# Optimization experiments

Measured on AMD Instinct MI355X. Metric: run time of the kernel, lower is better.

The kernel has to match this reference:

```python
import jax, jax.numpy as jnp
import numpy as np

D_MODEL = 1024
N_HEADS = 16
D_K = D_MODEL // N_HEADS


def setup_inputs() -> dict:
    key = jax.random.key(0)
    ks = jax.random.split(key, 10)
    s = 1.0 / np.sqrt(D_MODEL)
    def lin(k):
        kw, kb = jax.random.split(k)
        W = jax.random.uniform(kw, (D_MODEL, D_MODEL), jnp.float32, -s, s)
        b = jax.random.uniform(kb, (D_MODEL,), jnp.float32, -s, s)
        return W, b
    Wq, bq = lin(ks[0])
    Wk, bk = lin(ks[1])
    Wv, bv = lin(ks[2])
    Wo, bo = lin(ks[3])
    x = jax.random.normal(ks[4], (2, 2048, D_MODEL), jnp.float32)
    gamma = jnp.ones((D_MODEL,), jnp.float32)
    beta = jnp.zeros((D_MODEL,), jnp.float32)
    return {"x": x, "Wq": Wq, "bq": bq, "Wk": Wk, "bk": bk,
            "Wv": Wv, "bv": bv, "Wo": Wo, "bo": bo,
            "gamma": gamma, "beta": beta}


def _mha(x, Wq, bq, Wk, bk, Wv, bv, Wo, bo, gamma, beta):
    B, S, _ = x.shape
    residual = x
    # Linear uses y = x @ W.T + b (torch nn.Linear convention)
    q = (x @ Wq.T + bq).reshape(B, S, N_HEADS, D_K).transpose(0, 2, 1, 3)
    k = (x @ Wk.T + bk).reshape(B, S, N_HEADS, D_K).transpose(0, 2, 1, 3)
    v = (x @ Wv.T + bv).reshape(B, S, N_HEADS, D_K).transpose(0, 2, 1, 3)
    scores = jnp.einsum("bhqd,bhkd->bhqk", q, k) / jnp.sqrt(jnp.float32(D_K))
    attn = jax.nn.softmax(scores, axis=-1)
    out = jnp.einsum("bhqk,bhkd->bhqd", attn, v)
    out = out.transpose(0, 2, 1, 3).reshape(B, S, D_MODEL)
    out = out @ Wo.T + bo
    h = out + residual
    mu = jnp.mean(h, axis=-1, keepdims=True)
    var = jnp.var(h, axis=-1, keepdims=True)
    h = (h - mu) / jnp.sqrt(var + 1e-5) * gamma + beta
    return jnp.where(h >= 0, h, 0.01 * h)


def reference(x, Wq, bq, Wk, bk, Wv, bv, Wo, bo, gamma, beta):
    return _mha(x, Wq, bq, Wk, bk, Wv, bv, Wo, bo, gamma, beta)
```

## Files before the change

### kernel.cpp

```cpp
#include <hip/hip_runtime.h>

#define DM   1024
#define NH   16
#define DK   64
#define SEQ  2048
#define BATCH 2

typedef __attribute__((ext_vector_type(8))) short bf16x8;
typedef __attribute__((ext_vector_type(4))) float f32x4;

__device__ __forceinline__ unsigned short f2bf(float f) {
    unsigned int u = __builtin_bit_cast(unsigned int, f);
    u += 0x7FFFu + ((u >> 16) & 1u);
    return (unsigned short)(u >> 16);
}

__global__ __launch_bounds__(256)
void cvt_kernel(const float* __restrict__ x,
                const float* __restrict__ wq, const float* __restrict__ wk,
                const float* __restrict__ wv, const float* __restrict__ wo,
                unsigned short* __restrict__ xb,
                unsigned short* __restrict__ wqkvb,
                unsigned short* __restrict__ wob)
{
    const int seg = blockIdx.y;
    const float* src;
    unsigned short* dst;
    int n;
    if (seg == 0)      { src = x;  dst = xb;                  n = 4 << 20; }
    else if (seg == 1) { src = wq; dst = wqkvb;               n = 1 << 20; }
    else if (seg == 2) { src = wk; dst = wqkvb + (1 << 20);   n = 1 << 20; }
    else if (seg == 3) { src = wv; dst = wqkvb + (2 << 20);   n = 1 << 20; }
    else               { src = wo; dst = wob;                 n = 1 << 20; }
    for (int i = (blockIdx.x * 256 + threadIdx.x) * 4; i < n; i += 1024 * 256 * 4) {
        const float4 v = *reinterpret_cast<const float4*>(&src[i]);
        ushort4 o;
        o.x = f2bf(v.x); o.y = f2bf(v.y); o.z = f2bf(v.z); o.w = f2bf(v.w);
        *reinterpret_cast<ushort4*>(&dst[i]) = o;
    }
}

template <int MODE, int BN>
__global__ __launch_bounds__(256)
void gemm2_kernel(const unsigned short* __restrict__ Ab,
                  const unsigned short* __restrict__ Wall,
                  const float* __restrict__ B0, const float* __restrict__ B1,
                  const float* __restrict__ B2,
                  unsigned short* __restrict__ q_ws,
                  unsigned short* __restrict__ k_ws,
                  unsigned short* __restrict__ vt_ws,
                  const float* __restrict__ resid,
                  float* __restrict__ h_ws)
{
    __shared__ unsigned short sA[128 * 32];
    __shared__ unsigned short sB[BN * 32];

    const int tid = threadIdx.x, lane = tid & 63, wid = tid >> 6;
    const int n0 = blockIdx.x * BN, m0 = blockIdx.y * 128;
    const int z  = (MODE == 0) ? blockIdx.z : 0;
    const unsigned short* W = Wall + (size_t)z * (1 << 20);
    const float* bias = (MODE == 0) ? (z == 0 ? B0 : (z == 1 ? B1 : B2)) : B0;

    const int g = lane >> 4, lq = lane & 15;
    const int wr = wid >> 1, wc = wid & 1;
    const int rA = lane >> 2;
    const int csh = (lane & 3) * 8;

    f32x4 acc[4][BN / 32] = {};

    for (int k0 = 0; k0 < DM; k0 += 32) {
        #pragma unroll
        for (int i = 0; i < 2; ++i) {
            const int c = wid * 2 + i;
            __builtin_amdgcn_global_load_lds(
                (const __attribute__((address_space(1))) unsigned int*)
                    &Ab[(size_t)(m0 + c * 16 + rA) * DM + k0 + csh],
                (__attribute__((address_space(3))) unsigned int*)&sA[c * 512],
                16, 0, 0);
        }
        #pragma unroll
        for (int i = 0; i < BN / 64; ++i) {
            const int c = wid * (BN / 64) + i;
            __builtin_amdgcn_global_load_lds(
                (const __attribute__((address_space(1))) unsigned int*)
                    &W[(size_t)(n0 + c * 16 + rA) * DM + k0 + csh],
                (__attribute__((address_space(3))) unsigned int*)&sB[c * 512],
                16, 0, 0);
        }
        __syncthreads();

        bf16x8 a[4], b[BN / 32];
        #pragma unroll
        for (int m = 0; m < 4; ++m)
            a[m] = *reinterpret_cast<const bf16x8*>(&sA[(wr * 64 + m * 16 + lq) * 32 + 8 * g]);
        #pragma unroll
        for (int n = 0; n < BN / 32; ++n)
            b[n] = *reinterpret_cast<const bf16x8*>(&sB[(wc * (BN / 2) + n * 16 + lq) * 32 + 8 * g]);
        #pragma unroll
        for (int m = 0; m < 4; ++m)
            #pragma unroll
            for (int n = 0; n < BN / 32; ++n)
                acc[m][n] = __builtin_amdgcn_mfma_f32_16x16x32_bf16(
                    a[m], b[n], acc[m][n], 0, 0, 0);
        __syncthreads();
    }

    #pragma unroll
    for (int m = 0; m < 4; ++m) {
        #pragma unroll
        for (int n = 0; n < BN / 32; ++n) {
            #pragma unroll
            for (int j = 0; j < 4; ++j) {
                const int row = m0 + wr * 64 + m * 16 + 4 * g + j;
                const int col = n0 + wc * (BN / 2) + n * 16 + lq;
                float v = acc[m][n][j] + bias[col];
                if constexpr (MODE == 0) {
                    const int b_ = row >> 11, s = row & (SEQ - 1);
                    const int hh = col >> 6,  d = col & (DK - 1);
                    if (z == 0)
                        q_ws[(((size_t)(b_ * NH + hh) * SEQ + s) << 6) + d] = f2bf(v * 0.18033688f);
                    else if (z == 1)
                        k_ws[(((size_t)(b_ * NH + hh) * SEQ + s) << 6) + d] = f2bf(v);
                    else
                        vt_ws[((size_t)(b_ * NH + hh) * DK + d) * SEQ + s] = f2bf(v);
                } else {
                    const size_t idx = (size_t)row * DM + col;
                    h_ws[idx] = v + resid[idx];
                }
            }
        }
    }
}

__global__ __launch_bounds__(512)
void attn_kernel(const unsigned short* __restrict__ q_ws,
                 const unsigned short* __restrict__ k_ws,
                 const unsigned short* __restrict__ vt_ws,
                 unsigned short* __restrict__ ao_ws)
{
    __shared__ unsigned short lds4[4][4096];

    const int tid = threadIdx.x;
    const int lane = tid & 63, wid = tid >> 6;
    const int g = lane >> 4, lq = lane & 15;
    const int bh = blockIdx.y;
    const int q0 = blockIdx.x * 128;

    const size_t qbase = ((size_t)bh * SEQ + q0 + wid * 16 + lq) * DK;
    const bf16x8 aq0 = *reinterpret_cast<const bf16x8*>(&q_ws[qbase + 8 * g]);
    const bf16x8 aq1 = *reinterpret_cast<const bf16x8*>(&q_ws[qbase + 32 + 8 * g]);

    const short one_bf = (short)0x3F80;
    const bf16x8 onesf = {one_bf, one_bf, one_bf, one_bf, one_bf, one_bf, one_bf, one_bf};

    const int l8 = lane >> 3, l7 = lane & 7;
    const int scol = 8 * (l7 ^ l8);
    const int r7 = lq & 7;
    const int ck0 = 8 * (g ^ r7);
    const int ck1 = 8 * ((4 + g) ^ r7);

    const unsigned short* kp = &k_ws [((size_t)bh * SEQ + wid * 8 + l8) * DK + scol];
    const unsigned short* vp = &vt_ws[((size_t)bh * DK  + wid * 8 + l8) * SEQ + scol];

    const unsigned short* pK0 = &lds4[0][lq * 64 + ck0];
    const unsigned short* pK1 = &lds4[0][lq * 64 + ck1];
    const unsigned short* pV0 = &lds4[2][lq * 64 + ck0];
    const unsigned short* pV1 = &lds4[2][lq * 64 + ck1];

    f32x4 oacc[4] = {};
    f32x4 lacc = {};

    const int dst = wid * 512;

    auto stage = [&](int kbuf) {
        __builtin_amdgcn_global_load_lds(
            (const __attribute__((address_space(1))) unsigned int*)kp,
            (__attribute__((address_space(3))) unsigned int*)&lds4[kbuf][dst], 16, 0, 0);
        __builtin_amdgcn_global_load_lds(
            (const __attribute__((address_space(1))) unsigned int*)vp,
            (__attribute__((address_space(3))) unsigned int*)&lds4[2 + kbuf][dst], 16, 0, 0);
        kp += 64 * DK;
        vp += 64;
    };

    auto compute = [&](int OFF) {
        f32x4 st[4];
        __builtin_amdgcn_s_setprio(1);
        #pragma unroll
        for (int kb = 0; kb < 4; ++kb) {
            const bf16x8 k0 = *reinterpret_cast<const bf16x8*>(pK0 + OFF + kb * 1024);
            const bf16x8 k1 = *reinterpret_cast<const bf16x8*>(pK1 + OFF + kb * 1024);
            f32x4 zz = {};
            zz = __builtin_amdgcn_mfma_f32_16x16x32_bf16(k0, aq0, zz, 0, 0, 0);
            zz = __builtin_amdgcn_mfma_f32_16x16x32_bf16(k1, aq1, zz, 0, 0, 0);
            st[kb] = zz;
        }
        __builtin_amdgcn_s_setprio(0);

        unsigned int pk[4][2];
        #pragma unroll
        for (int kb = 0; kb < 4; ++kb) {
            float e0 = exp2f(st[kb][0]);
            float e1 = exp2f(st[kb][1]);
            float e2 = exp2f(st[kb][2]);
            float e3 = exp2f(st[kb][3]);
            asm("v_cvt_pk_bf16_f32 %0, %1, %2" : "=v"(pk[kb][0]) : "v"(e0), "v"(e1));
            asm("v_cvt_pk_bf16_f32 %0, %1, %2" : "=v"(pk[kb][1]) : "v"(e2), "v"(e3));
        }

        const int s01 = ((2 * g) & 3) * 16 + lq;
        const int s23 = ((2 * g + 1) & 3) * 16 + lq;
        const bool hi = (g >= 2);
        bf16x8 pf[2];
        #pragma unroll
        for (int m = 0; m < 2; ++m) {
            const unsigned int w0A = __shfl(pk[2 * m][0], s01), w0B = __shfl(pk[2 * m + 1][0], s01);
            const unsigned int w1A = __shfl(pk[2 * m][1], s01), w1B = __shfl(pk[2 * m + 1][1], s01);
            const unsigned int w2A = __shfl(pk[2 * m][0], s23), w2B = __shfl(pk[2 * m + 1][0], s23);
            const unsigned int w3A = __shfl(pk[2 * m][1], s23), w3B = __shfl(pk[2 * m + 1][1], s23);
            uint4 ww;
            ww.x = hi ? w0B : w0A;
            ww.y = hi ? w1B : w1A;
            ww.z = hi ? w2B : w2A;
            ww.w = hi ? w3B : w3A;
            pf[m] = __builtin_bit_cast(bf16x8, ww);
        }

        __builtin_amdgcn_s_setprio(1);
        lacc = __builtin_amdgcn_mfma_f32_16x16x32_bf16(onesf, pf[0], lacc, 0, 0, 0);
        lacc = __builtin_amdgcn_mfma_f32_16x16x32_bf16(onesf, pf[1], lacc, 0, 0, 0);
        #pragma unroll
        for (int db = 0; db < 4; ++db) {
            const bf16x8 v0 = *reinterpret_cast<const bf16x8*>(pV0 + OFF + db * 1024);
            const bf16x8 v1 = *reinterpret_cast<const bf16x8*>(pV1 + OFF + db * 1024);
            oacc[db] = __builtin_amdgcn_mfma_f32_16x16x32_bf16(v0, pf[0], oacc[db], 0, 0, 0);
            oacc[db] = __builtin_amdgcn_mfma_f32_16x16x32_bf16(v1, pf[1], oacc[db], 0, 0, 0);
        }
        __builtin_amdgcn_s_setprio(0);
    };

    stage(0);
    __syncthreads();

    for (int tt = 0; tt < 16; ++tt) {
        stage(1);
        compute(0);
        __syncthreads();
        if (tt < 15) stage(0);
        compute(4096);
        __syncthreads();
    }

    const int b_ = bh >> 4, hh = bh & 15;
    const int qg = q0 + wid * 16 + lq;
    const float rl = 1.0f / lacc[0];
    #pragma unroll
    for (int db = 0; db < 4; ++db) {
        ushort4 o;
        o.x = f2bf(oacc[db][0] * rl);
        o.y = f2bf(oacc[db][1] * rl);
        o.z = f2bf(oacc[db][2] * rl);
        o.w = f2bf(oacc[db][3] * rl);
        *reinterpret_cast<ushort4*>(
            &ao_ws[(size_t)(b_ * SEQ + qg) * DM + hh * 64 + db * 16 + 4 * g]) = o;
    }
}

__global__ __launch_bounds__(256)
void ln_kernel(const float* __restrict__ h, const float* __restrict__ gamma,
               const float* __restrict__ beta, float* __restrict__ out)
{
    __shared__ float s1[4], s2[4];
    const int row = blockIdx.x, tid = threadIdx.x;
    const float4 v = reinterpret_cast<const float4*>(h + (size_t)row * DM)[tid];
    float sum = v.x + v.y + v.z + v.w;
    float sq  = v.x * v.x + v.y * v.y + v.z * v.z + v.w * v.w;
    #pragma unroll
    for (int mk = 1; mk <= 32; mk <<= 1) {
        sum += __shfl_xor(sum, mk);
        sq  += __shfl_xor(sq, mk);
    }
    if ((tid & 63) == 0) { s1[tid >> 6] = sum; s2[tid >> 6] = sq; }
    __syncthreads();
    sum = s1[0] + s1[1] + s1[2] + s1[3];
    sq  = s2[0] + s2[1] + s2[2] + s2[3];
    const float mu = sum * (1.f / DM);
    const float var = sq * (1.f / DM) - mu * mu;
    const float rstd = rsqrtf(var + 1e-5f);
    const float4 gv = reinterpret_cast<const float4*>(gamma)[tid];
    const float4 bv = reinterpret_cast<const float4*>(beta)[tid];
    float4 o;
    o.x = (v.x - mu) * rstd * gv.x + bv.x;
    o.y = (v.y - mu) * rstd * gv.y + bv.y;
    o.z = (v.z - mu) * rstd * gv.z + bv.z;
    o.w = (v.w - mu) * rstd * gv.w + bv.w;
    o.x = o.x >= 0.f ? o.x : 0.01f * o.x;
    o.y = o.y >= 0.f ? o.y : 0.01f * o.y;
    o.z = o.z >= 0.f ? o.z : 0.01f * o.z;
    o.w = o.w >= 0.f ? o.w : 0.01f * o.w;
    reinterpret_cast<float4*>(out + (size_t)row * DM)[tid] = o;
}

extern "C" void kernel_launch(void* const* d_in, const int* in_sizes, int n_in,
                              void* d_out, int out_size, void* d_ws, size_t ws_size,
                              hipStream_t stream)
{
    const float* x     = (const float*)d_in[0];
    const float* Wq    = (const float*)d_in[1];
    const float* bq    = (const float*)d_in[2];
    const float* Wk    = (const float*)d_in[3];
    const float* bk    = (const float*)d_in[4];
    const float* Wv    = (const float*)d_in[5];
    const float* bv    = (const float*)d_in[6];
    const float* Wo    = (const float*)d_in[7];
    const float* bo    = (const float*)d_in[8];
    const float* gamma = (const float*)d_in[9];
    const float* beta  = (const float*)d_in[10];

    char* ws = (char*)d_ws;
    unsigned short* q_ws   = (unsigned short*)(ws);
    unsigned short* k_ws   = (unsigned short*)(ws + (8u << 20));
    unsigned short* vt_ws  = (unsigned short*)(ws + (16u << 20));
    unsigned short* ao_ws  = (unsigned short*)(ws + (24u << 20));
    unsigned short* xb_ws  = (unsigned short*)(ws + (32u << 20));
    unsigned short* wqkv_b = (unsigned short*)(ws + (40u << 20));
    unsigned short* wo_b   = (unsigned short*)(ws + (46u << 20));
    float* h_ws = (float*)ws;

    const dim3 blk(256);
    cvt_kernel<<<dim3(1024, 5), blk, 0, stream>>>(
        x, Wq, Wk, Wv, Wo, xb_ws, wqkv_b, wo_b);
    gemm2_kernel<0, 128><<<dim3(8, 32, 3), blk, 0, stream>>>(
        xb_ws, wqkv_b, bq, bk, bv, q_ws, k_ws, vt_ws, nullptr, nullptr);
    attn_kernel<<<dim3(16, 32), dim3(512), 0, stream>>>(q_ws, k_ws, vt_ws, ao_ws);
    gemm2_kernel<1, 64><<<dim3(16, 32, 1), blk, 0, stream>>>(
        ao_ws, wo_b, bo, nullptr, nullptr, nullptr, nullptr, nullptr, x, h_ws);
    ln_kernel<<<dim3(4096), blk, 0, stream>>>(h_ws, gamma, beta, (float*)d_out);
}
```

Measured before the change: 138.7 us.

## Deepen attention K/V LDS pipeline to four stages with vmcnt-gated barriers

The attention kernel's K/V shared-memory staging grows from a double buffer to a four-slot ring, with two tiles always in flight ahead of compute. Each step now uses an explicit s_waitcnt vmcnt plus a bare s_barrier instead of two __syncthreads per loop iteration, and the loop is unrolled by four with a peeled tail. The aim is to hide global-to-LDS load latency behind the MFMA work and to halve the barrier count. In exchange, LDS per block doubles to 64KB, which may cut the number of resident blocks per CU.

```diff
diff --git a/kernel.cpp b/kernel.cpp
--- a/kernel.cpp
+++ b/kernel.cpp
@@ -138,7 +138,7 @@
                  const unsigned short* __restrict__ vt_ws,
                  unsigned short* __restrict__ ao_ws)
 {
-    __shared__ unsigned short lds4[4][4096];
+    __shared__ unsigned short lds4[8][4096];
 
     const int tid = threadIdx.x;
     const int lane = tid & 63, wid = tid >> 6;
@@ -164,8 +164,8 @@
 
     const unsigned short* pK0 = &lds4[0][lq * 64 + ck0];
     const unsigned short* pK1 = &lds4[0][lq * 64 + ck1];
-    const unsigned short* pV0 = &lds4[2][lq * 64 + ck0];
-    const unsigned short* pV1 = &lds4[2][lq * 64 + ck1];
+    const unsigned short* pV0 = &lds4[4][lq * 64 + ck0];
+    const unsigned short* pV1 = &lds4[4][lq * 64 + ck1];
 
     f32x4 oacc[4] = {};
     f32x4 lacc = {};
@@ -178,7 +178,7 @@
             (__attribute__((address_space(3))) unsigned int*)&lds4[kbuf][dst], 16, 0, 0);
         __builtin_amdgcn_global_load_lds(
             (const __attribute__((address_space(1))) unsigned int*)vp,
-            (__attribute__((address_space(3))) unsigned int*)&lds4[2 + kbuf][dst], 16, 0, 0);
+            (__attribute__((address_space(3))) unsigned int*)&lds4[4 + kbuf][dst], 16, 0, 0);
         kp += 64 * DK;
         vp += 64;
     };
@@ -240,16 +240,42 @@
     };
 
     stage(0);
-    __syncthreads();
-
-    for (int tt = 0; tt < 16; ++tt) {
+    stage(1);
+
+    #pragma unroll 1
+    for (int tt = 0; tt < 7; ++tt) {
+        stage(2);
+        asm volatile("s_waitcnt vmcnt(4)" ::: "memory");
+        __builtin_amdgcn_s_barrier();
+        compute(0);
+        stage(3);
+        asm volatile("s_waitcnt vmcnt(4)" ::: "memory");
+        __builtin_amdgcn_s_barrier();
+        compute(4096);
+        stage(0);
+        asm volatile("s_waitcnt vmcnt(4)" ::: "memory");
+        __builtin_amdgcn_s_barrier();
+        compute(8192);
         stage(1);
-        compute(0);
-        __syncthreads();
-        if (tt < 15) stage(0);
-        compute(4096);
-        __syncthreads();
-    }
+        asm volatile("s_waitcnt vmcnt(4)" ::: "memory");
+        __builtin_amdgcn_s_barrier();
+        compute(12288);
+    }
+
+    stage(2);
+    asm volatile("s_waitcnt vmcnt(4)" ::: "memory");
+    __builtin_amdgcn_s_barrier();
+    compute(0);
+    stage(3);
+    asm volatile("s_waitcnt vmcnt(4)" ::: "memory");
+    __builtin_amdgcn_s_barrier();
+    compute(4096);
+    asm volatile("s_waitcnt vmcnt(2)" ::: "memory");
+    __builtin_amdgcn_s_barrier();
+    compute(8192);
+    asm volatile("s_waitcnt vmcnt(0)" ::: "memory");
+    __builtin_amdgcn_s_barrier();
+    compute(12288);
 
     const int b_ = bh >> 4, hh = bh & 15;
     const int qg = q0 + wid * 16 + lq;
```

New measurement: 140.9 us. No clear change (+1.6%).

## Split attention over two key halves and merge partial outputs in a combine kernel

Applied to the files above, without the earlier changes.

The attention kernel now splits the key sequence into two halves along a new grid dimension, so it launches twice as many blocks. Each block writes a normalized partial output plus its softmax denominator to workspace. A new combine kernel blends the two partials using the denominators and writes the final attention output. The aim is more parallelism and better CU load balance; the cost is an extra launch and an extra round trip of bf16 partials through memory. The workspace reuse relies on the x/weight bf16 buffers being dead by the time attention runs.

```diff
diff --git a/kernel.cpp b/kernel.cpp
--- a/kernel.cpp
+++ b/kernel.cpp
@@ -13,6 +13,9 @@
     unsigned int u = __builtin_bit_cast(unsigned int, f);
     u += 0x7FFFu + ((u >> 16) & 1u);
     return (unsigned short)(u >> 16);
+}
+__device__ __forceinline__ float bf2f(unsigned short u) {
+    return __builtin_bit_cast(float, ((unsigned int)u) << 16);
 }
 
 __global__ __launch_bounds__(256)
@@ -136,7 +139,8 @@
 void attn_kernel(const unsigned short* __restrict__ q_ws,
                  const unsigned short* __restrict__ k_ws,
                  const unsigned short* __restrict__ vt_ws,
-                 unsigned short* __restrict__ ao_ws)
+                 unsigned short* __restrict__ po_ws,
+                 float* __restrict__ pl_ws)
 {
     __shared__ unsigned short lds4[4][4096];
 
@@ -145,6 +149,8 @@
     const int g = lane >> 4, lq = lane & 15;
     const int bh = blockIdx.y;
     const int q0 = blockIdx.x * 128;
+    const int z  = blockIdx.z;
+    const int kt0 = z * 1024;
 
     const size_t qbase = ((size_t)bh * SEQ + q0 + wid * 16 + lq) * DK;
     const bf16x8 aq0 = *reinterpret_cast<const bf16x8*>(&q_ws[qbase + 8 * g]);
@@ -159,8 +165,8 @@
     const int ck0 = 8 * (g ^ r7);
     const int ck1 = 8 * ((4 + g) ^ r7);
 
-    const unsigned short* kp = &k_ws [((size_t)bh * SEQ + wid * 8 + l8) * DK + scol];
-    const unsigned short* vp = &vt_ws[((size_t)bh * DK  + wid * 8 + l8) * SEQ + scol];
+    const unsigned short* kp = &k_ws [((size_t)bh * SEQ + kt0 + wid * 8 + l8) * DK + scol];
+    const unsigned short* vp = &vt_ws[((size_t)bh * DK  + wid * 8 + l8) * SEQ + kt0 + scol];
 
     const unsigned short* pK0 = &lds4[0][lq * 64 + ck0];
     const unsigned short* pK1 = &lds4[0][lq * 64 + ck1];
@@ -242,11 +248,11 @@
     stage(0);
     __syncthreads();
 
-    for (int tt = 0; tt < 16; ++tt) {
+    for (int tt = 0; tt < 8; ++tt) {
         stage(1);
         compute(0);
         __syncthreads();
-        if (tt < 15) stage(0);
+        if (tt < 7) stage(0);
         compute(4096);
         __syncthreads();
     }
@@ -254,6 +260,7 @@
     const int b_ = bh >> 4, hh = bh & 15;
     const int qg = q0 + wid * 16 + lq;
     const float rl = 1.0f / lacc[0];
+    unsigned short* po = po_ws + (size_t)z * (4u << 20);
     #pragma unroll
     for (int db = 0; db < 4; ++db) {
         ushort4 o;
@@ -262,8 +269,33 @@
         o.z = f2bf(oacc[db][2] * rl);
         o.w = f2bf(oacc[db][3] * rl);
         *reinterpret_cast<ushort4*>(
-            &ao_ws[(size_t)(b_ * SEQ + qg) * DM + hh * 64 + db * 16 + 4 * g]) = o;
-    }
+            &po[(size_t)(b_ * SEQ + qg) * DM + hh * 64 + db * 16 + 4 * g]) = o;
+    }
+    if (g == 0)
+        pl_ws[z * (NH * BATCH * SEQ) + bh * SEQ + qg] = lacc[0];
+}
+
+__global__ __launch_bounds__(256)
+void combine_kernel(const unsigned short* po, const float* pl,
+                    unsigned short* ao)
+{
+    const int idx4 = blockIdx.x * 256 + threadIdx.x;
+    const int flat = idx4 * 4;
+    const int r  = flat >> 10;
+    const int b_ = r >> 11, s = r & (SEQ - 1);
+    const int hh = (flat >> 6) & 15;
+    const int pli = (b_ * NH + hh) * SEQ + s;
+    const float l0 = pl[pli], l1 = pl[NH * BATCH * SEQ + pli];
+    const float w0 = l0 / (l0 + l1);
+    const float w1 = 1.0f - w0;
+    const ushort4 a0 = reinterpret_cast<const ushort4*>(po)[idx4];
+    const ushort4 a1 = reinterpret_cast<const ushort4*>(po + (4u << 20))[idx4];
+    ushort4 o;
+    o.x = f2bf(w0 * bf2f(a0.x) + w1 * bf2f(a1.x));
+    o.y = f2bf(w0 * bf2f(a0.y) + w1 * bf2f(a1.y));
+    o.z = f2bf(w0 * bf2f(a0.z) + w1 * bf2f(a1.z));
+    o.w = f2bf(w0 * bf2f(a0.w) + w1 * bf2f(a1.w));
+    reinterpret_cast<ushort4*>(ao)[idx4] = o;
 }
 
 __global__ __launch_bounds__(256)
@@ -322,8 +354,10 @@
     unsigned short* k_ws   = (unsigned short*)(ws + (8u << 20));
     unsigned short* vt_ws  = (unsigned short*)(ws + (16u << 20));
     unsigned short* ao_ws  = (unsigned short*)(ws + (24u << 20));
+    unsigned short* po_ws  = (unsigned short*)(ws + (24u << 20));
     unsigned short* xb_ws  = (unsigned short*)(ws + (32u << 20));
     unsigned short* wqkv_b = (unsigned short*)(ws + (40u << 20));
+    float*          pl_ws  = (float*)(ws + (40u << 20));
     unsigned short* wo_b   = (unsigned short*)(ws + (46u << 20));
     float* h_ws = (float*)ws;
 
@@ -332,7 +366,9 @@
         x, Wq, Wk, Wv, Wo, xb_ws, wqkv_b, wo_b);
     gemm2_kernel<0, 128><<<dim3(8, 32, 3), blk, 0, stream>>>(
         xb_ws, wqkv_b, bq, bk, bv, q_ws, k_ws, vt_ws, nullptr, nullptr);
-    attn_kernel<<<dim3(16, 32), dim3(512), 0, stream>>>(q_ws, k_ws, vt_ws, ao_ws);
+    attn_kernel<<<dim3(16, 32, 2), dim3(512), 0, stream>>>(
+        q_ws, k_ws, vt_ws, po_ws, pl_ws);
+    combine_kernel<<<dim3(8192), blk, 0, stream>>>(po_ws, pl_ws, ao_ws);
     gemm2_kernel<1, 64><<<dim3(16, 32, 1), blk, 0, stream>>>(
         ao_ws, wo_b, bo, nullptr, nullptr, nullptr, nullptr, nullptr, x, h_ws);
     ln_kernel<<<dim3(4096), blk, 0, stream>>>(h_ws, gamma, beta, (float*)d_out);
```

Result: slower. 151.5 us (+9.2%).
